# Optimization experiments

Hardware: AMD Instinct MI355X
Metric: run time of the kernel (lower is better)

Reference implementation:

```python
import jax, jax.numpy as jnp
import numpy as np

N = 50000          # number of input points
M = 1024           # num_supernodes
SPACE = 3          # space_dim
FUN = 5            # fun_dim
C = 256            # channel_dim
RADIUS = 0.05      # ball-query radius (pos in unit cube)


def setup_inputs() -> dict:
    key = jax.random.key(0)
    k1, k2, k3, k4, k5 = jax.random.split(key, 5)
    pos = jax.random.uniform(k1, (N, SPACE), jnp.float32)          # unit cube coords
    fun = jax.random.normal(k2, (N, FUN), jnp.float32)             # physical fields
    supernode_idx = jax.random.randint(k3, (M,), 0, N)             # sampled supernodes
    W = jax.random.normal(k4, (C, SPACE + FUN), jnp.float32) / np.sqrt(SPACE + FUN)
    b = jax.random.normal(k5, (C,), jnp.float32) * 0.01
    return {"pos": pos, "fun": fun, "supernode_idx": supernode_idx, "W": W, "b": b}


def reference(pos, fun, supernode_idx, W, b):
    # enc_proj on every point: [N, SPACE+FUN] @ [SPACE+FUN, C] -> [N, C]
    x = jnp.concatenate([pos, fun], axis=-1) @ W.T + b
    # gather supernode positions: [M, SPACE]
    sp = pos[supernode_idx]
    # squared pairwise distances supernode->point: [M, N]
    d2 = jnp.sum((sp[:, None, :] - pos[None, :, :]) ** 2, axis=-1)
    mask = (d2 <= RADIUS * RADIUS).astype(x.dtype)        # radius_graph neighborhood
    cnt = jnp.maximum(mask.sum(axis=-1, keepdims=True), 1.0)
    # mean-aggregate projected point features onto each supernode: [M, C]
    latent = (mask @ x) / cnt
    return latent
```

## Files before the change

kernel.cpp:

```cpp
#include <hip/hip_runtime.h>


#define NC 20
#define NCELLS (NC * NC * NC)
#define SLOTS 64
#define POISON 0xAAAAAAAAu

__device__ __forceinline__ unsigned decode_count(unsigned raw) {
    return (raw >= 0x80000000u) ? raw - POISON : raw;
}

__global__ __launch_bounds__(256) void sn_scatter(
    const float* __restrict__ pos, const float* __restrict__ fun,
    int* __restrict__ cnt, float* __restrict__ rec, int N)
{
    int i = blockIdx.x * 256 + (int)threadIdx.x;
    if (i >= N) return;
    float px = pos[i * 3 + 0], py = pos[i * 3 + 1], pz = pos[i * 3 + 2];
    int cx = min(NC - 1, (int)(px * (float)NC));
    int cy = min(NC - 1, (int)(py * (float)NC));
    int cz = min(NC - 1, (int)(pz * (float)NC));
    int c = (cz * NC + cy) * NC + cx;
    unsigned k = decode_count((unsigned)atomicAdd(cnt + c, 1));
    if (k < SLOTS) {
        float* r = rec + ((size_t)c * SLOTS + k) * 8;
        *(float4*)r       = make_float4(px, py, pz, fun[i * 5 + 0]);
        *(float4*)(r + 4) = make_float4(fun[i * 5 + 1], fun[i * 5 + 2],
                                        fun[i * 5 + 3], fun[i * 5 + 4]);
    }
}

__global__ __launch_bounds__(256) void sn_accum(
    const float* __restrict__ pos, const int* __restrict__ sidx,
    const int* __restrict__ cnt, const float* __restrict__ rec,
    const float* __restrict__ W, const float* __restrict__ bias,
    float* __restrict__ out, int M)
{
    const int lane = (int)threadIdx.x & 63;
    const int m = blockIdx.x * 4 + ((int)threadIdx.x >> 6);
    if (m >= M) return;

    const int idx = sidx[m];
    const float sx = pos[idx * 3 + 0];
    const float sy = pos[idx * 3 + 1];
    const float sz = pos[idx * 3 + 2];

    const float PAD = 0.050001f;
    int cx0 = max(0, (int)floorf((sx - PAD) * (float)NC));
    int cx1 = min(NC - 1, (int)floorf((sx + PAD) * (float)NC));
    int cy0 = max(0, (int)floorf((sy - PAD) * (float)NC));
    int cy1 = min(NC - 1, (int)floorf((sy + PAD) * (float)NC));
    int cz0 = max(0, (int)floorf((sz - PAD) * (float)NC));
    int cz1 = min(NC - 1, (int)floorf((sz + PAD) * (float)NC));
    int nx = cx1 - cx0 + 1, ny = cy1 - cy0 + 1, nz = cz1 - cz0 + 1;
    int ncell = nx * ny * nz;

    int cj = 0, base = 0;
    if (lane < ncell) {
        int jx = lane % nx, jr = lane / nx;
        int jy = jr % ny,   jz = jr / ny;
        int c = ((cz0 + jz) * NC + (cy0 + jy)) * NC + (cx0 + jx);
        cj = min((int)decode_count((unsigned)cnt[c]), SLOTS);
        base = c * SLOTS;
    }

    int incl = cj;
#pragma unroll
    for (int d = 1; d < 64; d <<= 1) {
        int v = __shfl_up(incl, d);
        if (lane >= d) incl += v;
    }
    const int excl = incl - cj;
    const int T = __shfl(incl, 63);

    float s0 = 0, s1 = 0, s2 = 0, s3 = 0, s4 = 0, s5 = 0, s6 = 0, s7 = 0, sc = 0;
    const float R2 = 0.0025f;

    for (int t0 = 0; t0 < T; t0 += 64) {
        const int t = t0 + lane;
        const bool act = t < T;
        const int tt = act ? t : 0;
        int lo = 0;
#pragma unroll
        for (int s = 32; s; s >>= 1) {
            int v = __shfl(incl, lo + s - 1);
            if (v <= tt) lo += s;
        }
        const int ridx = __shfl(base, lo) + (tt - __shfl(excl, lo));
        const float* r = rec + (size_t)ridx * 8;
        const float4 a  = *(const float4*)r;
        const float4 b4 = *(const float4*)(r + 4);
        float dx = __fsub_rn(sx, a.x);
        float dy = __fsub_rn(sy, a.y);
        float dz = __fsub_rn(sz, a.z);
        float d2 = __fadd_rn(__fadd_rn(__fmul_rn(dx, dx), __fmul_rn(dy, dy)),
                             __fmul_rn(dz, dz));
        if (act && d2 <= R2) {
            s0 += a.x;  s1 += a.y;  s2 += a.z;  s3 += a.w;
            s4 += b4.x; s5 += b4.y; s6 += b4.z; s7 += b4.w; sc += 1.0f;
        }
    }

#pragma unroll
    for (int d = 32; d; d >>= 1) {
        s0 += __shfl_xor(s0, d); s1 += __shfl_xor(s1, d); s2 += __shfl_xor(s2, d);
        s3 += __shfl_xor(s3, d); s4 += __shfl_xor(s4, d); s5 += __shfl_xor(s5, d);
        s6 += __shfl_xor(s6, d); s7 += __shfl_xor(s7, d); sc += __shfl_xor(sc, d);
    }

    const int c0 = lane * 4;
    float4 o = make_float4(0.f, 0.f, 0.f, 0.f);
    if (sc > 0.0f) {
        const float inv = 1.0f / sc;
        const float f0 = s0 * inv, f1 = s1 * inv, f2 = s2 * inv, f3 = s3 * inv;
        const float f4 = s4 * inv, f5 = s5 * inv, f6 = s6 * inv, f7 = s7 * inv;
        const float4 bb = *(const float4*)(bias + c0);
        float acc[4];
#pragma unroll
        for (int rr = 0; rr < 4; ++rr) {
            const float* w = W + (size_t)(c0 + rr) * 8;
            const float4 w0 = *(const float4*)w;
            const float4 w1 = *(const float4*)(w + 4);
            acc[rr] = f0 * w0.x + f1 * w0.y + f2 * w0.z + f3 * w0.w
                    + f4 * w1.x + f5 * w1.y + f6 * w1.z + f7 * w1.w;
        }
        o = make_float4(bb.x + acc[0], bb.y + acc[1], bb.z + acc[2], bb.w + acc[3]);
    }
    *(float4*)(out + (size_t)m * 256 + c0) = o;
}

extern "C" void kernel_launch(void* const* d_in, const int* in_sizes, int n_in,
                              void* d_out, int out_size, void* d_ws, size_t ws_size,
                              hipStream_t stream) {
    const float* pos  = (const float*)d_in[0];
    const float* fun  = (const float*)d_in[1];
    const int*   sidx = (const int*)d_in[2];
    const float* W    = (const float*)d_in[3];
    const float* b    = (const float*)d_in[4];
    float* out = (float*)d_out;

    const int N = in_sizes[0] / 3;
    const int M = in_sizes[2];

    int*   cnt = (int*)d_ws;
    float* rec = (float*)((char*)d_ws + 32768);

    sn_scatter<<<(N + 255) / 256, 256, 0, stream>>>(pos, fun, cnt, rec, N);
    sn_accum<<<(M + 3) / 4, 256, 0, stream>>>(pos, sidx, cnt, rec, W, b, out, M);
}
```

Baseline: 71.72 us.

## Split each supernode's candidate scan across two wavefronts with software prefetch

Each supernode is now handled by two wavefronts that take alternating 64-candidate chunks. Their partial sums are combined through shared memory, and the 256-channel projection is then spread over all 128 threads. The candidate loop loads the next chunk before processing the current one, to hide memory latency. This doubles the block count and adds a block barrier and a small shared-memory reduction.

```diff
diff --git a/kernel.cpp b/kernel.cpp
--- a/kernel.cpp
+++ b/kernel.cpp
@@ -36,97 +36,136 @@
     const float* __restrict__ W, const float* __restrict__ bias,
     float* __restrict__ out, int M)
 {
-    const int lane = (int)threadIdx.x & 63;
-    const int m = blockIdx.x * 4 + ((int)threadIdx.x >> 6);
-    if (m >= M) return;
+    const int tid  = (int)threadIdx.x;
+    const int lane = tid & 63;
+    const int wl   = (tid >> 6) & 1;
+    const int ls   = tid >> 7;
+    const int m    = blockIdx.x * 2 + ls;
 
-    const int idx = sidx[m];
-    const float sx = pos[idx * 3 + 0];
-    const float sy = pos[idx * 3 + 1];
-    const float sz = pos[idx * 3 + 2];
-
-    const float PAD = 0.050001f;
-    int cx0 = max(0, (int)floorf((sx - PAD) * (float)NC));
-    int cx1 = min(NC - 1, (int)floorf((sx + PAD) * (float)NC));
-    int cy0 = max(0, (int)floorf((sy - PAD) * (float)NC));
-    int cy1 = min(NC - 1, (int)floorf((sy + PAD) * (float)NC));
-    int cz0 = max(0, (int)floorf((sz - PAD) * (float)NC));
-    int cz1 = min(NC - 1, (int)floorf((sz + PAD) * (float)NC));
-    int nx = cx1 - cx0 + 1, ny = cy1 - cy0 + 1, nz = cz1 - cz0 + 1;
-    int ncell = nx * ny * nz;
-
-    int cj = 0, base = 0;
-    if (lane < ncell) {
-        int jx = lane % nx, jr = lane / nx;
-        int jy = jr % ny,   jz = jr / ny;
-        int c = ((cz0 + jz) * NC + (cy0 + jy)) * NC + (cx0 + jx);
-        cj = min((int)decode_count((unsigned)cnt[c]), SLOTS);
-        base = c * SLOTS;
-    }
-
-    int incl = cj;
-#pragma unroll
-    for (int d = 1; d < 64; d <<= 1) {
-        int v = __shfl_up(incl, d);
-        if (lane >= d) incl += v;
-    }
-    const int excl = incl - cj;
-    const int T = __shfl(incl, 63);
+    __shared__ float part[2][2][12];
 
     float s0 = 0, s1 = 0, s2 = 0, s3 = 0, s4 = 0, s5 = 0, s6 = 0, s7 = 0, sc = 0;
-    const float R2 = 0.0025f;
 
-    for (int t0 = 0; t0 < T; t0 += 64) {
-        const int t = t0 + lane;
-        const bool act = t < T;
-        const int tt = act ? t : 0;
-        int lo = 0;
+    if (m < M) {
+        const int idx = sidx[m];
+        const float sx = pos[idx * 3 + 0];
+        const float sy = pos[idx * 3 + 1];
+        const float sz = pos[idx * 3 + 2];
+
+        const float PAD = 0.050001f;
+        int cx0 = max(0, (int)floorf((sx - PAD) * (float)NC));
+        int cx1 = min(NC - 1, (int)floorf((sx + PAD) * (float)NC));
+        int cy0 = max(0, (int)floorf((sy - PAD) * (float)NC));
+        int cy1 = min(NC - 1, (int)floorf((sy + PAD) * (float)NC));
+        int cz0 = max(0, (int)floorf((sz - PAD) * (float)NC));
+        int cz1 = min(NC - 1, (int)floorf((sz + PAD) * (float)NC));
+        int nx = cx1 - cx0 + 1, ny = cy1 - cy0 + 1, nz = cz1 - cz0 + 1;
+        int ncell = nx * ny * nz;
+
+        int cj = 0, base = 0;
+        if (lane < ncell) {
+            int jx = lane % nx, jr = lane / nx;
+            int jy = jr % ny,   jz = jr / ny;
+            int c = ((cz0 + jz) * NC + (cy0 + jy)) * NC + (cx0 + jx);
+            cj = min((int)decode_count((unsigned)cnt[c]), SLOTS);
+            base = c * SLOTS;
+        }
+
+        int incl = cj;
 #pragma unroll
-        for (int s = 32; s; s >>= 1) {
-            int v = __shfl(incl, lo + s - 1);
-            if (v <= tt) lo += s;
+        for (int d = 1; d < 64; d <<= 1) {
+            int v = __shfl_up(incl, d);
+            if (lane >= d) incl += v;
         }
-        const int ridx = __shfl(base, lo) + (tt - __shfl(excl, lo));
-        const float* r = rec + (size_t)ridx * 8;
-        const float4 a  = *(const float4*)r;
-        const float4 b4 = *(const float4*)(r + 4);
-        float dx = __fsub_rn(sx, a.x);
-        float dy = __fsub_rn(sy, a.y);
-        float dz = __fsub_rn(sz, a.z);
-        float d2 = __fadd_rn(__fadd_rn(__fmul_rn(dx, dx), __fmul_rn(dy, dy)),
-                             __fmul_rn(dz, dz));
-        if (act && d2 <= R2) {
-            s0 += a.x;  s1 += a.y;  s2 += a.z;  s3 += a.w;
-            s4 += b4.x; s5 += b4.y; s6 += b4.z; s7 += b4.w; sc += 1.0f;
+        const int excl = incl - cj;
+        const int T = __shfl(incl, 63);
+
+        const float R2 = 0.0025f;
+
+        auto searchLoad = [&](int tt, float4& a, float4& b4) {
+            int lo = 0;
+#pragma unroll
+            for (int s = 32; s; s >>= 1) {
+                int v = __shfl(incl, lo + s - 1);
+                if (v <= tt) lo += s;
+            }
+            const int ridx = __shfl(base, lo) + (tt - __shfl(excl, lo));
+            const float* r = rec + (size_t)ridx * 8;
+            a  = *(const float4*)r;
+            b4 = *(const float4*)(r + 4);
+        };
+
+        int t0 = wl * 64;
+        if (t0 < T) {
+            bool act = (t0 + lane) < T;
+            float4 ca, cb;
+            searchLoad(act ? t0 + lane : 0, ca, cb);
+            for (t0 += 128;; t0 += 128) {
+                const bool more = t0 < T;
+                float4 na, nb;
+                bool actn = false;
+                if (more) {
+                    actn = (t0 + lane) < T;
+                    searchLoad(actn ? t0 + lane : 0, na, nb);
+                }
+                float dx = __fsub_rn(sx, ca.x);
+                float dy = __fsub_rn(sy, ca.y);
+                float dz = __fsub_rn(sz, ca.z);
+                float d2 = __fadd_rn(__fadd_rn(__fmul_rn(dx, dx), __fmul_rn(dy, dy)),
+                                     __fmul_rn(dz, dz));
+                if (act && d2 <= R2) {
+                    s0 += ca.x; s1 += ca.y; s2 += ca.z; s3 += ca.w;
+                    s4 += cb.x; s5 += cb.y; s6 += cb.z; s7 += cb.w; sc += 1.0f;
+                }
+                if (!more) break;
+                ca = na; cb = nb; act = actn;
+            }
+        }
+
+#pragma unroll
+        for (int d = 32; d; d >>= 1) {
+            s0 += __shfl_xor(s0, d); s1 += __shfl_xor(s1, d); s2 += __shfl_xor(s2, d);
+            s3 += __shfl_xor(s3, d); s4 += __shfl_xor(s4, d); s5 += __shfl_xor(s5, d);
+            s6 += __shfl_xor(s6, d); s7 += __shfl_xor(s7, d); sc += __shfl_xor(sc, d);
+        }
+        if (lane == 0) {
+            part[ls][wl][0] = s0; part[ls][wl][1] = s1; part[ls][wl][2] = s2;
+            part[ls][wl][3] = s3; part[ls][wl][4] = s4; part[ls][wl][5] = s5;
+            part[ls][wl][6] = s6; part[ls][wl][7] = s7; part[ls][wl][8] = sc;
         }
     }
+    __syncthreads();
 
-#pragma unroll
-    for (int d = 32; d; d >>= 1) {
-        s0 += __shfl_xor(s0, d); s1 += __shfl_xor(s1, d); s2 += __shfl_xor(s2, d);
-        s3 += __shfl_xor(s3, d); s4 += __shfl_xor(s4, d); s5 += __shfl_xor(s5, d);
-        s6 += __shfl_xor(s6, d); s7 += __shfl_xor(s7, d); sc += __shfl_xor(sc, d);
+    const int g  = tid >> 7;
+    const int mm = blockIdx.x * 2 + g;
+    if (mm < M) {
+        const int c0 = (tid & 127) * 2;
+        const float tc = part[g][0][8] + part[g][1][8];
+        float o0 = 0.f, o1 = 0.f;
+        if (tc > 0.0f) {
+            const float inv = 1.0f / tc;
+            const float f0 = (part[g][0][0] + part[g][1][0]) * inv;
+            const float f1 = (part[g][0][1] + part[g][1][1]) * inv;
+            const float f2 = (part[g][0][2] + part[g][1][2]) * inv;
+            const float f3 = (part[g][0][3] + part[g][1][3]) * inv;
+            const float f4 = (part[g][0][4] + part[g][1][4]) * inv;
+            const float f5 = (part[g][0][5] + part[g][1][5]) * inv;
+            const float f6 = (part[g][0][6] + part[g][1][6]) * inv;
+            const float f7 = (part[g][0][7] + part[g][1][7]) * inv;
+            const float* w0p = W + (size_t)c0 * 8;
+            const float4 w00 = *(const float4*)w0p;
+            const float4 w01 = *(const float4*)(w0p + 4);
+            const float4 w10 = *(const float4*)(w0p + 8);
+            const float4 w11 = *(const float4*)(w0p + 12);
+            o0 = bias[c0]
+               + f0 * w00.x + f1 * w00.y + f2 * w00.z + f3 * w00.w
+               + f4 * w01.x + f5 * w01.y + f6 * w01.z + f7 * w01.w;
+            o1 = bias[c0 + 1]
+               + f0 * w10.x + f1 * w10.y + f2 * w10.z + f3 * w10.w
+               + f4 * w11.x + f5 * w11.y + f6 * w11.z + f7 * w11.w;
+        }
+        *(float2*)(out + (size_t)mm * 256 + c0) = make_float2(o0, o1);
     }
-
-    const int c0 = lane * 4;
-    float4 o = make_float4(0.f, 0.f, 0.f, 0.f);
-    if (sc > 0.0f) {
-        const float inv = 1.0f / sc;
-        const float f0 = s0 * inv, f1 = s1 * inv, f2 = s2 * inv, f3 = s3 * inv;
-        const float f4 = s4 * inv, f5 = s5 * inv, f6 = s6 * inv, f7 = s7 * inv;
-        const float4 bb = *(const float4*)(bias + c0);
-        float acc[4];
-#pragma unroll
-        for (int rr = 0; rr < 4; ++rr) {
-            const float* w = W + (size_t)(c0 + rr) * 8;
-            const float4 w0 = *(const float4*)w;
-            const float4 w1 = *(const float4*)(w + 4);
-            acc[rr] = f0 * w0.x + f1 * w0.y + f2 * w0.z + f3 * w0.w
-                    + f4 * w1.x + f5 * w1.y + f6 * w1.z + f7 * w1.w;
-        }
-        o = make_float4(bb.x + acc[0], bb.y + acc[1], bb.z + acc[2], bb.w + acc[3]);
-    }
-    *(float4*)(out + (size_t)m * 256 + c0) = o;
 }
 
 extern "C" void kernel_launch(void* const* d_in, const int* in_sizes, int n_in,
@@ -146,5 +185,5 @@
     float* rec = (float*)((char*)d_ws + 32768);
 
     sn_scatter<<<(N + 255) / 256, 256, 0, stream>>>(pos, fun, cnt, rec, N);
-    sn_accum<<<(M + 3) / 4, 256, 0, stream>>>(pos, sidx, cnt, rec, W, b, out, M);
+    sn_accum<<<(M + 1) / 2, 256, 0, stream>>>(pos, sidx, cnt, rec, W, b, out, M);
 }
```

New measurement: 70.12 us. 2.2% less time.
